# Optimization experiments

Measured on AMD Instinct MI355X. Metric: run time of the kernel, lower is better.

The kernel has to match this reference:

```python
import jax, jax.numpy as jnp
import numpy as np

B, S, D, H = 512, 512, 64, 128  # batch, seq_len, input_size, hidden_size


def setup_inputs() -> dict:
    key = jax.random.key(0)
    ks = jax.random.split(key, 12)
    s_in = 1.0 / np.sqrt(H)
    def u(k, shape):
        return jax.random.uniform(k, shape, jnp.float32, -s_in, s_in)
    return {
        "x": jax.random.normal(ks[0], (B, S, D), jnp.float32),
        # layer 0 (PyTorch gate order i,f,g,o stacked along first dim)
        "W_ih0": u(ks[1], (4 * H, D)),
        "W_hh0": u(ks[2], (4 * H, H)),
        "b_ih0": u(ks[3], (4 * H,)),
        "b_hh0": u(ks[4], (4 * H,)),
        # layer 1
        "W_ih1": u(ks[5], (4 * H, H)),
        "W_hh1": u(ks[6], (4 * H, H)),
        "b_ih1": u(ks[7], (4 * H,)),
        "b_hh1": u(ks[8], (4 * H,)),
        # linear head hidden -> 1
        "W_lin": u(ks[9], (1, H)),
        "b_lin": u(ks[10], (1,)),
    }


def _lstm_layer(x, W_ih, W_hh, b_ih, b_hh):
    # x: [B, S, Din] -> h sequence [B, S, H]
    b, s, _ = x.shape
    h_dim = W_hh.shape[1]
    # precompute input contribution for all timesteps (the compute-heavy GEMM)
    pre = jnp.einsum('bsd,gd->bsg', x, W_ih) + (b_ih + b_hh)  # [B, S, 4H]

    def step(carry, p_t):
        h, c = carry
        gates = p_t + h @ W_hh.T  # [B, 4H]
        i, f, g, o = jnp.split(gates, 4, axis=-1)
        i = jax.nn.sigmoid(i)
        f = jax.nn.sigmoid(f)
        g = jnp.tanh(g)
        o = jax.nn.sigmoid(o)
        c = f * c + i * g
        h = o * jnp.tanh(c)
        return (h, c), h

    h0 = jnp.zeros((b, h_dim), x.dtype)
    (_, _), hs = jax.lax.scan(step, (h0, h0), pre.transpose(1, 0, 2))
    return hs.transpose(1, 0, 2)  # [B, S, H]


def reference(x, W_ih0, W_hh0, b_ih0, b_hh0, W_ih1, W_hh1, b_ih1, b_hh1, W_lin, b_lin):
    h1 = _lstm_layer(x, W_ih0, W_hh0, b_ih0, b_hh0)
    h2 = _lstm_layer(h1, W_ih1, W_hh1, b_ih1, b_hh1)
    last = h2[:, -1, :]  # [B, H]
    return last @ W_lin.T + b_lin  # [B, 1]
```

## Files before the change

kernel.cpp:

```cpp
#include <hip/hip_runtime.h>

typedef _Float16 half8 __attribute__((ext_vector_type(8)));
typedef _Float16 half4 __attribute__((ext_vector_type(4)));
typedef _Float16 half2v __attribute__((ext_vector_type(2)));
typedef float floatx4 __attribute__((ext_vector_type(4)));

__device__ __forceinline__ float fast_rcp(float x) { return __builtin_amdgcn_rcpf(x); }
__device__ __forceinline__ float fast_sigmoid(float x) {
  return fast_rcp(1.f + __expf(-x));
}
__device__ __forceinline__ float fast_tanh(float x) {
  return 1.f - 2.f * fast_rcp(1.f + __expf(2.f * x));
}

__global__ void prep_kernel(const float* __restrict__ wih0, const float* __restrict__ whh0,
                            const float* __restrict__ bih0, const float* __restrict__ bhh0,
                            const float* __restrict__ wih1, const float* __restrict__ whh1,
                            const float* __restrict__ bih1, const float* __restrict__ bhh1,
                            _Float16* __restrict__ w0f, _Float16* __restrict__ w1f,
                            float* __restrict__ bias0, float* __restrict__ bias1)
{
  int stride = gridDim.x * blockDim.x;
  int idx0 = blockIdx.x * blockDim.x + threadIdx.x;
  const int N0 = 6*32*64*8;
  const int N1 = 8*32*64*8;
  for (int e = idx0; e < N0 + N1 + 1024; e += stride) {
    if (e < N0) {
      int j = e & 7; int le = e >> 3; int lane = le & 63; int frag = le >> 6;
      int kt = frag >> 5, ntile = frag & 31;
      int n = ntile*16 + (lane & 15);
      int kk = kt*32 + ((lane >> 4) << 3) + j;
      float v = (kk < 64) ? wih0[n*64 + kk] : whh0[n*128 + (kk - 64)];
      w0f[e] = (_Float16)v;
    } else if (e < N0 + N1) {
      int e2 = e - N0;
      int j = e2 & 7; int le = e2 >> 3; int lane = le & 63; int frag = le >> 6;
      int kt = frag >> 5, ntile = frag & 31;
      int n = ntile*16 + (lane & 15);
      int kk = kt*32 + ((lane >> 4) << 3) + j;
      float v = (kk < 128) ? wih1[n*128 + kk] : whh1[n*128 + (kk - 128)];
      w1f[e2] = (_Float16)v;
    } else {
      int i = e - (N0 + N1);
      if (i < 512) bias0[i] = bih0[i] + bhh0[i];
      else         bias1[i - 512] = bih1[i - 512] + bhh1[i - 512];
    }
  }
}


__global__ __launch_bounds__(512, 2) void lstm_l0(const float* __restrict__ x,
    const _Float16* __restrict__ w0f, const float* __restrict__ bias0,
    _Float16* __restrict__ h1out)
{
  const int tid = threadIdx.x;
  const int lane = tid & 63;
  const int w = tid >> 6;
  const int r0 = blockIdx.x * 2;

  __shared__ float preLDS[2][8192];
  __shared__ half8 aF[2][2*64];
  __shared__ half8 hA[2][4*8];
  __shared__ _Float16 hist[16][2][128];

  for (int i = tid; i < 2*4*8*4; i += 512) ((int*)hA)[i] = 0;

  half8 bf[6][4];
#pragma unroll
  for (int kt = 0; kt < 6; ++kt)
#pragma unroll
    for (int g = 0; g < 4; ++g) {
      int frag = kt*32 + (g*8 + w);
      bf[kt][g] = *reinterpret_cast<const half8*>(w0f + (size_t)(frag*64 + lane)*8);
      asm volatile("" : "+a"(bf[kt][g]));
    }
  float bias_v[4];
#pragma unroll
  for (int g = 0; g < 4; ++g) bias_v[g] = bias0[g*128 + w*16 + (lane & 15)];

  const int sdt = tid >> 6, sr = (tid >> 5) & 1, scp = (tid & 31) * 2;
  const int sm = sdt*2 + sr;
  const int sidx = ((scp>>5)*64 + sm + (((scp&31)>>3)<<4))*8 + (scp & 7);

  const bool arow = (lane & 11) == 0;
  const int cIdx = ((lane >> 4) << 1) | ((lane >> 2) & 1);
  const int rb = lane >> 4;
  const int en = w*16 + (lane & 15);
  const int eoff = ((en>>5)*8 + ((en&31)>>3)*2 + rb)*8 + (en&7);
  float cst = 0.f;

  {
    float2 v0 = *reinterpret_cast<const float2*>(x + ((size_t)(r0+sr)*512 + sdt)*64 + scp);
    float2 v1 = *reinterpret_cast<const float2*>(x + ((size_t)(r0+sr)*512 + 8 + sdt)*64 + scp);
    half2v h0; h0[0] = (_Float16)v0.x; h0[1] = (_Float16)v0.y;
    half2v h1v; h1v[0] = (_Float16)v1.x; h1v[1] = (_Float16)v1.y;
    *reinterpret_cast<half2v*>(((_Float16*)aF[0]) + sidx) = h0;
    *reinterpret_cast<half2v*>(((_Float16*)aF[1]) + sidx) = h1v;
  }
  __syncthreads();
  {
    floatx4 accP[4];
#pragma unroll
    for (int g = 0; g < 4; ++g) { float bb = bias_v[g]; accP[g] = (floatx4){bb,bb,bb,bb}; }
#pragma unroll
    for (int kt = 0; kt < 2; ++kt) {
      half8 af = aF[0][kt*64 + lane];
#pragma unroll
      for (int g = 0; g < 4; ++g)
        accP[g] = __builtin_amdgcn_mfma_f32_16x16x32_f16(af, bf[kt][g], accP[g], 0, 0, 0);
    }
#pragma unroll
    for (int reg = 0; reg < 4; ++reg) {
      int m = ((lane>>4)<<2) + reg;
      floatx4 pv = (floatx4){accP[0][reg], accP[1][reg], accP[2][reg], accP[3][reg]};
      *reinterpret_cast<floatx4*>(&preLDS[0][(m*128 + en)*4]) = pv;
    }
  }
  __syncthreads();

  half8 a2 = {}, a3 = {}, a4 = {}, a5 = {};

  for (int t = 0; t < 512; ++t) {
    const int b = t >> 3;
    if ((t & 7) == 0 && b < 62) {
      int s = (b+2)*8 + sdt;
      float2 v = *reinterpret_cast<const float2*>(x + ((size_t)(r0+sr)*512 + s)*64 + scp);
      half2v hv; hv[0] = (_Float16)v.x; hv[1] = (_Float16)v.y;
      *reinterpret_cast<half2v*>(((_Float16*)aF[b&1]) + sidx) = hv;
    }
    __syncthreads();
    if ((t & 7) == 0) {
      if (t != 0) {
        int tbase = t - 8;
        int fr = tid >> 8, rest = tid & 255;
        int fdt = rest >> 5, n = (rest & 31) * 4;
        half4 v = *reinterpret_cast<const half4*>(&hist[(tbase + fdt) & 15][fr][n]);
        *reinterpret_cast<half4*>(h1out + ((size_t)(r0 + fr)*512 + tbase + fdt)*128 + n) = v;
      }
      if (b < 63) {
        int slot = (b+1) & 1;
        floatx4 accP[4];
#pragma unroll
        for (int g = 0; g < 4; ++g) { float bb = bias_v[g]; accP[g] = (floatx4){bb,bb,bb,bb}; }
#pragma unroll
        for (int kt = 0; kt < 2; ++kt) {
          half8 af = aF[slot][kt*64 + lane];
#pragma unroll
          for (int g = 0; g < 4; ++g)
            accP[g] = __builtin_amdgcn_mfma_f32_16x16x32_f16(af, bf[kt][g], accP[g], 0, 0, 0);
        }
#pragma unroll
        for (int reg = 0; reg < 4; ++reg) {
          int m = ((lane>>4)<<2) + reg;
          floatx4 pv = (floatx4){accP[0][reg], accP[1][reg], accP[2][reg], accP[3][reg]};
          *reinterpret_cast<floatx4*>(&preLDS[slot][(m*128 + en)*4]) = pv;
        }
      }
    }

    floatx4 p4 = (floatx4){0.f, 0.f, 0.f, 0.f};
    if (lane < 32) {
      int mstep = ((t & 7) << 1) + rb;
      p4 = *reinterpret_cast<const floatx4*>(&preLDS[b & 1][(mstep*128 + en)*4]);
    }
    floatx4 acc[4];
#pragma unroll
    for (int g = 0; g < 4; ++g) acc[g] = (floatx4){p4[g], 0.f, 0.f, 0.f};

    const int cur = t & 1;
    if (arow) {
      a2 = hA[cur][0*8 + cIdx];
      a3 = hA[cur][1*8 + cIdx];
      a4 = hA[cur][2*8 + cIdx];
      a5 = hA[cur][3*8 + cIdx];
    }
#pragma unroll
    for (int g = 0; g < 4; ++g)
      acc[g] = __builtin_amdgcn_mfma_f32_16x16x32_f16(a2, bf[2][g], acc[g], 0, 0, 0);
#pragma unroll
    for (int g = 0; g < 4; ++g)
      acc[g] = __builtin_amdgcn_mfma_f32_16x16x32_f16(a3, bf[3][g], acc[g], 0, 0, 0);
#pragma unroll
    for (int g = 0; g < 4; ++g)
      acc[g] = __builtin_amdgcn_mfma_f32_16x16x32_f16(a4, bf[4][g], acc[g], 0, 0, 0);
#pragma unroll
    for (int g = 0; g < 4; ++g)
      acc[g] = __builtin_amdgcn_mfma_f32_16x16x32_f16(a5, bf[5][g], acc[g], 0, 0, 0);

    if (lane < 32) {
      float ii = fast_sigmoid(acc[0][0]);
      float ff = fast_sigmoid(acc[1][0]);
      float gg = fast_tanh(acc[2][0]);
      float oo = fast_sigmoid(acc[3][0]);
      cst = ff*cst + ii*gg;
      float hv2 = oo*fast_tanh(cst);
      _Float16 hh = (_Float16)hv2;
      ((_Float16*)hA[cur^1])[eoff] = hh;
      hist[t & 15][rb][en] = hh;
    }
  }
  __syncthreads();
  {
    int tbase = 504;
    int fr = tid >> 8, rest = tid & 255;
    int fdt = rest >> 5, n = (rest & 31) * 4;
    half4 v = *reinterpret_cast<const half4*>(&hist[(tbase + fdt) & 15][fr][n]);
    *reinterpret_cast<half4*>(h1out + ((size_t)(r0 + fr)*512 + tbase + fdt)*128 + n) = v;
  }
}

__global__ __launch_bounds__(512, 2) void lstm_l1(const _Float16* __restrict__ h1in,
    const _Float16* __restrict__ w1f, const float* __restrict__ bias1,
    const float* __restrict__ wlin, const float* __restrict__ blin,
    float* __restrict__ out)
{
  const int tid = threadIdx.x;
  const int lane = tid & 63;
  const int w = tid >> 6;
  const int r0 = blockIdx.x * 2;

  __shared__ float preLDS[2][8192];
  __shared__ half8 aF[2][4*64];
  __shared__ half8 hA[2][4*8];
  __shared__ float head[256];

  for (int i = tid; i < 2*4*8*4; i += 512) ((int*)hA)[i] = 0;

  half8 bf[8][4];
#pragma unroll
  for (int kt = 0; kt < 8; ++kt)
#pragma unroll
    for (int g = 0; g < 4; ++g) {
      int frag = kt*32 + (g*8 + w);
      bf[kt][g] = *reinterpret_cast<const half8*>(w1f + (size_t)(frag*64 + lane)*8);
      asm volatile("" : "+a"(bf[kt][g]));
    }
  float bias_v[4];
#pragma unroll
  for (int g = 0; g < 4; ++g) bias_v[g] = bias1[g*128 + w*16 + (lane & 15)];

  const int sdt = tid >> 6, sr = (tid >> 5) & 1, scq = (tid & 31) * 4;
  const int sm = sdt*2 + sr;
  const int sidx = ((scq>>5)*64 + sm + (((scq&31)>>3)<<4))*8 + (scq & 7);

  const bool arow = (lane & 11) == 0;
  const int cIdx = ((lane >> 4) << 1) | ((lane >> 2) & 1);
  const int rb = lane >> 4;
  const int en = w*16 + (lane & 15);
  const int eoff = ((en>>5)*8 + ((en&31)>>3)*2 + rb)*8 + (en&7);
  const float wl = (lane < 32) ? wlin[en] : 0.f;
  float cst = 0.f;
  float hl = 0.f;

  {
    uint2 v0 = *reinterpret_cast<const uint2*>(h1in + ((size_t)(r0+sr)*512 + sdt)*128 + scq);
    uint2 v1 = *reinterpret_cast<const uint2*>(h1in + ((size_t)(r0+sr)*512 + 8 + sdt)*128 + scq);
    *reinterpret_cast<uint2*>(((_Float16*)aF[0]) + sidx) = v0;
    *reinterpret_cast<uint2*>(((_Float16*)aF[1]) + sidx) = v1;
  }
  __syncthreads();
  {
    floatx4 accP[4];
#pragma unroll
    for (int g = 0; g < 4; ++g) { float bb = bias_v[g]; accP[g] = (floatx4){bb,bb,bb,bb}; }
#pragma unroll
    for (int kt = 0; kt < 4; ++kt) {
      half8 af = aF[0][kt*64 + lane];
#pragma unroll
      for (int g = 0; g < 4; ++g)
        accP[g] = __builtin_amdgcn_mfma_f32_16x16x32_f16(af, bf[kt][g], accP[g], 0, 0, 0);
    }
#pragma unroll
    for (int reg = 0; reg < 4; ++reg) {
      int m = ((lane>>4)<<2) + reg;
      floatx4 pv = (floatx4){accP[0][reg], accP[1][reg], accP[2][reg], accP[3][reg]};
      *reinterpret_cast<floatx4*>(&preLDS[0][(m*128 + en)*4]) = pv;
    }
  }
  __syncthreads();

  half8 a4 = {}, a5 = {}, a6 = {}, a7 = {};

  for (int t = 0; t < 512; ++t) {
    const int b = t >> 3;
    if ((t & 7) == 0 && b < 62) {
      int s = (b+2)*8 + sdt;
      uint2 v = *reinterpret_cast<const uint2*>(h1in + ((size_t)(r0+sr)*512 + s)*128 + scq);
      *reinterpret_cast<uint2*>(((_Float16*)aF[b&1]) + sidx) = v;
    }
    __syncthreads();
    if ((t & 7) == 0 && b < 63) {
      int slot = (b+1) & 1;
      floatx4 accP[4];
#pragma unroll
      for (int g = 0; g < 4; ++g) { float bb = bias_v[g]; accP[g] = (floatx4){bb,bb,bb,bb}; }
#pragma unroll
      for (int kt = 0; kt < 4; ++kt) {
        half8 af = aF[slot][kt*64 + lane];
#pragma unroll
        for (int g = 0; g < 4; ++g)
          accP[g] = __builtin_amdgcn_mfma_f32_16x16x32_f16(af, bf[kt][g], accP[g], 0, 0, 0);
      }
#pragma unroll
      for (int reg = 0; reg < 4; ++reg) {
        int m = ((lane>>4)<<2) + reg;
        floatx4 pv = (floatx4){accP[0][reg], accP[1][reg], accP[2][reg], accP[3][reg]};
        *reinterpret_cast<floatx4*>(&preLDS[slot][(m*128 + en)*4]) = pv;
      }
    }

    floatx4 p4 = (floatx4){0.f, 0.f, 0.f, 0.f};
    if (lane < 32) {
      int mstep = ((t & 7) << 1) + rb;
      p4 = *reinterpret_cast<const floatx4*>(&preLDS[b & 1][(mstep*128 + en)*4]);
    }
    floatx4 acc[4];
#pragma unroll
    for (int g = 0; g < 4; ++g) acc[g] = (floatx4){p4[g], 0.f, 0.f, 0.f};

    const int cur = t & 1;
    if (arow) {
      a4 = hA[cur][0*8 + cIdx];
      a5 = hA[cur][1*8 + cIdx];
      a6 = hA[cur][2*8 + cIdx];
      a7 = hA[cur][3*8 + cIdx];
    }
#pragma unroll
    for (int g = 0; g < 4; ++g)
      acc[g] = __builtin_amdgcn_mfma_f32_16x16x32_f16(a4, bf[4][g], acc[g], 0, 0, 0);
#pragma unroll
    for (int g = 0; g < 4; ++g)
      acc[g] = __builtin_amdgcn_mfma_f32_16x16x32_f16(a5, bf[5][g], acc[g], 0, 0, 0);
#pragma unroll
    for (int g = 0; g < 4; ++g)
      acc[g] = __builtin_amdgcn_mfma_f32_16x16x32_f16(a6, bf[6][g], acc[g], 0, 0, 0);
#pragma unroll
    for (int g = 0; g < 4; ++g)
      acc[g] = __builtin_amdgcn_mfma_f32_16x16x32_f16(a7, bf[7][g], acc[g], 0, 0, 0);

    if (lane < 32) {
      float ii = fast_sigmoid(acc[0][0]);
      float ff = fast_sigmoid(acc[1][0]);
      float gg = fast_tanh(acc[2][0]);
      float oo = fast_sigmoid(acc[3][0]);
      cst = ff*cst + ii*gg;
      hl = oo*fast_tanh(cst);
      ((_Float16*)hA[cur^1])[eoff] = (_Float16)hl;
    }
  }

  if (lane < 32) head[rb*128 + en] = hl * wl;
  __syncthreads();
  if (tid < 2) {
    float s = blin[0];
    for (int n = 0; n < 128; ++n) s += head[tid*128 + n];
    out[r0 + tid] = s;
  }
}

extern "C" void kernel_launch(void* const* d_in, const int* in_sizes, int n_in,
                              void* d_out, int out_size, void* d_ws, size_t ws_size,
                              hipStream_t stream)
{
  const float* x    = (const float*)d_in[0];
  const float* wih0 = (const float*)d_in[1];
  const float* whh0 = (const float*)d_in[2];
  const float* bih0 = (const float*)d_in[3];
  const float* bhh0 = (const float*)d_in[4];
  const float* wih1 = (const float*)d_in[5];
  const float* whh1 = (const float*)d_in[6];
  const float* bih1 = (const float*)d_in[7];
  const float* bhh1 = (const float*)d_in[8];
  const float* wlin = (const float*)d_in[9];
  const float* blin = (const float*)d_in[10];
  float* out = (float*)d_out;

  char* ws = (char*)d_ws;
  _Float16* w0f = (_Float16*)(ws);
  _Float16* w1f = (_Float16*)(ws + 196608);
  float* bias0  = (float*)(ws + 458752);
  float* bias1  = (float*)(ws + 460800);
  _Float16* h1  = (_Float16*)(ws + 1048576);

  prep_kernel<<<256, 256, 0, stream>>>(wih0, whh0, bih0, bhh0, wih1, whh1, bih1, bhh1,
                                       w0f, w1f, bias0, bias1);
  lstm_l0<<<256, 512, 0, stream>>>(x, w0f, bias0, h1);
  lstm_l1<<<256, 512, 0, stream>>>(h1, w1f, bias1, wlin, blin, out);
}
```

Measured before the change: 785.2 us.

## Unroll LSTM recurrence by 16 steps with compile-time slots and prefetched loads

The per-timestep loop in both LSTM layer kernels is restructured into windows of 8 steps, unrolled two at a time, so buffer slots and history indices become compile-time constants. The precomputed input-gate row for the next step is loaded from LDS early, before the activations, instead of at the start of each step. The global load of the next input chunk is issued before the window's compute and written to LDS only after a later barrier, hiding load latency behind the recurrence. Code size and register pressure grow, and the barrier placement changes the ordering of LDS writes and reads.

```diff
diff --git a/kernel.cpp b/kernel.cpp
--- a/kernel.cpp
+++ b/kernel.cpp
@@ -4,6 +4,8 @@
 typedef _Float16 half4 __attribute__((ext_vector_type(4)));
 typedef _Float16 half2v __attribute__((ext_vector_type(2)));
 typedef float floatx4 __attribute__((ext_vector_type(4)));
+
+template<int N> struct ic { static constexpr int value = N; };
 
 __device__ __forceinline__ float fast_rcp(float x) { return __builtin_amdgcn_rcpf(x); }
 __device__ __forceinline__ float fast_sigmoid(float x) {
@@ -48,7 +50,6 @@
   }
 }
 
-
 __global__ __launch_bounds__(512, 2) void lstm_l0(const float* __restrict__ x,
     const _Float16* __restrict__ w0f, const float* __restrict__ bias0,
     _Float16* __restrict__ h1out)
@@ -87,6 +88,8 @@
   const int rb = lane >> 4;
   const int en = w*16 + (lane & 15);
   const int eoff = ((en>>5)*8 + ((en&31)>>3)*2 + rb)*8 + (en&7);
+  const int fr = tid >> 8, rest = tid & 255;
+  const int fdt = rest >> 5, fn = (rest & 31) * 4;
   float cst = 0.f;
 
   {
@@ -116,78 +119,43 @@
       *reinterpret_cast<floatx4*>(&preLDS[0][(m*128 + en)*4]) = pv;
     }
   }
-  __syncthreads();
 
   half8 a2 = {}, a3 = {}, a4 = {}, a5 = {};
-
-  for (int t = 0; t < 512; ++t) {
-    const int b = t >> 3;
-    if ((t & 7) == 0 && b < 62) {
-      int s = (b+2)*8 + sdt;
-      float2 v = *reinterpret_cast<const float2*>(x + ((size_t)(r0+sr)*512 + s)*64 + scp);
-      half2v hv; hv[0] = (_Float16)v.x; hv[1] = (_Float16)v.y;
-      *reinterpret_cast<half2v*>(((_Float16*)aF[b&1]) + sidx) = hv;
-    }
-    __syncthreads();
-    if ((t & 7) == 0) {
-      if (t != 0) {
-        int tbase = t - 8;
-        int fr = tid >> 8, rest = tid & 255;
-        int fdt = rest >> 5, n = (rest & 31) * 4;
-        half4 v = *reinterpret_cast<const half4*>(&hist[(tbase + fdt) & 15][fr][n]);
-        *reinterpret_cast<half4*>(h1out + ((size_t)(r0 + fr)*512 + tbase + fdt)*128 + n) = v;
-      }
-      if (b < 63) {
-        int slot = (b+1) & 1;
-        floatx4 accP[4];
-#pragma unroll
-        for (int g = 0; g < 4; ++g) { float bb = bias_v[g]; accP[g] = (floatx4){bb,bb,bb,bb}; }
-#pragma unroll
-        for (int kt = 0; kt < 2; ++kt) {
-          half8 af = aF[slot][kt*64 + lane];
-#pragma unroll
-          for (int g = 0; g < 4; ++g)
-            accP[g] = __builtin_amdgcn_mfma_f32_16x16x32_f16(af, bf[kt][g], accP[g], 0, 0, 0);
-        }
-#pragma unroll
-        for (int reg = 0; reg < 4; ++reg) {
-          int m = ((lane>>4)<<2) + reg;
-          floatx4 pv = (floatx4){accP[0][reg], accP[1][reg], accP[2][reg], accP[3][reg]};
-          *reinterpret_cast<floatx4*>(&preLDS[slot][(m*128 + en)*4]) = pv;
-        }
-      }
-    }
-
-    floatx4 p4 = (floatx4){0.f, 0.f, 0.f, 0.f};
+  float2 sv;
+  floatx4 acc[4];
+#pragma unroll
+  for (int g = 0; g < 4; ++g) acc[g] = (floatx4){0.f,0.f,0.f,0.f};
+
+  floatx4 p4c = (floatx4){0.f,0.f,0.f,0.f};
+  if (lane < 32)
+    p4c = *reinterpret_cast<const floatx4*>(&preLDS[0][(rb*128 + en)*4]);
+
+  auto core = [&](auto tag) {
+    constexpr int TM = decltype(tag)::value;
+    constexpr int CUR = TM & 1;
+    constexpr int TN = (TM + 1) & 15;
+    if (arow) {
+      a2 = hA[CUR][ 0 + cIdx];
+      a3 = hA[CUR][ 8 + cIdx];
+      a4 = hA[CUR][16 + cIdx];
+      a5 = hA[CUR][24 + cIdx];
+    }
+    acc[0][0] = p4c[0]; acc[1][0] = p4c[1]; acc[2][0] = p4c[2]; acc[3][0] = p4c[3];
+#pragma unroll
+    for (int g = 0; g < 4; ++g)
+      acc[g] = __builtin_amdgcn_mfma_f32_16x16x32_f16(a2, bf[2][g], acc[g], 0, 0, 0);
+#pragma unroll
+    for (int g = 0; g < 4; ++g)
+      acc[g] = __builtin_amdgcn_mfma_f32_16x16x32_f16(a3, bf[3][g], acc[g], 0, 0, 0);
+#pragma unroll
+    for (int g = 0; g < 4; ++g)
+      acc[g] = __builtin_amdgcn_mfma_f32_16x16x32_f16(a4, bf[4][g], acc[g], 0, 0, 0);
+#pragma unroll
+    for (int g = 0; g < 4; ++g)
+      acc[g] = __builtin_amdgcn_mfma_f32_16x16x32_f16(a5, bf[5][g], acc[g], 0, 0, 0);
     if (lane < 32) {
-      int mstep = ((t & 7) << 1) + rb;
-      p4 = *reinterpret_cast<const floatx4*>(&preLDS[b & 1][(mstep*128 + en)*4]);
-    }
-    floatx4 acc[4];
-#pragma unroll
-    for (int g = 0; g < 4; ++g) acc[g] = (floatx4){p4[g], 0.f, 0.f, 0.f};
-
-    const int cur = t & 1;
-    if (arow) {
-      a2 = hA[cur][0*8 + cIdx];
-      a3 = hA[cur][1*8 + cIdx];
-      a4 = hA[cur][2*8 + cIdx];
-      a5 = hA[cur][3*8 + cIdx];
-    }
-#pragma unroll
-    for (int g = 0; g < 4; ++g)
-      acc[g] = __builtin_amdgcn_mfma_f32_16x16x32_f16(a2, bf[2][g], acc[g], 0, 0, 0);
-#pragma unroll
-    for (int g = 0; g < 4; ++g)
-      acc[g] = __builtin_amdgcn_mfma_f32_16x16x32_f16(a3, bf[3][g], acc[g], 0, 0, 0);
-#pragma unroll
-    for (int g = 0; g < 4; ++g)
-      acc[g] = __builtin_amdgcn_mfma_f32_16x16x32_f16(a4, bf[4][g], acc[g], 0, 0, 0);
-#pragma unroll
-    for (int g = 0; g < 4; ++g)
-      acc[g] = __builtin_amdgcn_mfma_f32_16x16x32_f16(a5, bf[5][g], acc[g], 0, 0, 0);
-
-    if (lane < 32) {
+      p4c = *reinterpret_cast<const floatx4*>(
+          &preLDS[TN >> 3][((((TN & 7) << 1) + rb)*128 + en)*4]);
       float ii = fast_sigmoid(acc[0][0]);
       float ff = fast_sigmoid(acc[1][0]);
       float gg = fast_tanh(acc[2][0]);
@@ -195,17 +163,62 @@
       cst = ff*cst + ii*gg;
       float hv2 = oo*fast_tanh(cst);
       _Float16 hh = (_Float16)hv2;
-      ((_Float16*)hA[cur^1])[eoff] = hh;
-      hist[t & 15][rb][en] = hh;
-    }
+      ((_Float16*)hA[CUR^1])[eoff] = hh;
+      hist[TM][rb][en] = hh;
+    }
+  };
+
+  auto window = [&](int B, auto slot_tag) {
+    constexpr int SLOT = decltype(slot_tag)::value;
+    __syncthreads();
+    if (B < 62)
+      sv = *reinterpret_cast<const float2*>(x + ((size_t)(r0+sr)*512 + (B+2)*8 + sdt)*64 + scp);
+    if (B >= 1) {
+      int tbase = (B-1)*8;
+      half4 v = *reinterpret_cast<const half4*>(&hist[((SLOT^1)<<3) + fdt][fr][fn]);
+      *reinterpret_cast<half4*>(h1out + ((size_t)(r0+fr)*512 + tbase + fdt)*128 + fn) = v;
+    }
+    if (B < 63) {
+      floatx4 accP[4];
+#pragma unroll
+      for (int g = 0; g < 4; ++g) { float bb = bias_v[g]; accP[g] = (floatx4){bb,bb,bb,bb}; }
+#pragma unroll
+      for (int kt = 0; kt < 2; ++kt) {
+        half8 af = aF[SLOT^1][kt*64 + lane];
+#pragma unroll
+        for (int g = 0; g < 4; ++g)
+          accP[g] = __builtin_amdgcn_mfma_f32_16x16x32_f16(af, bf[kt][g], accP[g], 0, 0, 0);
+      }
+#pragma unroll
+      for (int reg = 0; reg < 4; ++reg) {
+        int m = ((lane>>4)<<2) + reg;
+        floatx4 pv = (floatx4){accP[0][reg], accP[1][reg], accP[2][reg], accP[3][reg]};
+        *reinterpret_cast<floatx4*>(&preLDS[SLOT^1][(m*128 + en)*4]) = pv;
+      }
+    }
+    core(ic<SLOT*8 + 0>{});
+    __syncthreads();
+    if (B < 62) {
+      half2v hv; hv[0] = (_Float16)sv.x; hv[1] = (_Float16)sv.y;
+      *reinterpret_cast<half2v*>(((_Float16*)aF[SLOT]) + sidx) = hv;
+    }
+    core(ic<SLOT*8 + 1>{});
+    __syncthreads(); core(ic<SLOT*8 + 2>{});
+    __syncthreads(); core(ic<SLOT*8 + 3>{});
+    __syncthreads(); core(ic<SLOT*8 + 4>{});
+    __syncthreads(); core(ic<SLOT*8 + 5>{});
+    __syncthreads(); core(ic<SLOT*8 + 6>{});
+    __syncthreads(); core(ic<SLOT*8 + 7>{});
+  };
+
+  for (int bp = 0; bp < 32; ++bp) {
+    window(2*bp,     ic<0>{});
+    window(2*bp + 1, ic<1>{});
   }
   __syncthreads();
   {
-    int tbase = 504;
-    int fr = tid >> 8, rest = tid & 255;
-    int fdt = rest >> 5, n = (rest & 31) * 4;
-    half4 v = *reinterpret_cast<const half4*>(&hist[(tbase + fdt) & 15][fr][n]);
-    *reinterpret_cast<half4*>(h1out + ((size_t)(r0 + fr)*512 + tbase + fdt)*128 + n) = v;
+    half4 v = *reinterpret_cast<const half4*>(&hist[8 + fdt][fr][fn]);
+    *reinterpret_cast<half4*>(h1out + ((size_t)(r0+fr)*512 + 504 + fdt)*128 + fn) = v;
   }
 }
 
@@ -277,76 +290,92 @@
       *reinterpret_cast<floatx4*>(&preLDS[0][(m*128 + en)*4]) = pv;
     }
   }
-  __syncthreads();
 
   half8 a4 = {}, a5 = {}, a6 = {}, a7 = {};
-
-  for (int t = 0; t < 512; ++t) {
-    const int b = t >> 3;
-    if ((t & 7) == 0 && b < 62) {
-      int s = (b+2)*8 + sdt;
-      uint2 v = *reinterpret_cast<const uint2*>(h1in + ((size_t)(r0+sr)*512 + s)*128 + scq);
-      *reinterpret_cast<uint2*>(((_Float16*)aF[b&1]) + sidx) = v;
-    }
-    __syncthreads();
-    if ((t & 7) == 0 && b < 63) {
-      int slot = (b+1) & 1;
-      floatx4 accP[4];
-#pragma unroll
-      for (int g = 0; g < 4; ++g) { float bb = bias_v[g]; accP[g] = (floatx4){bb,bb,bb,bb}; }
-#pragma unroll
-      for (int kt = 0; kt < 4; ++kt) {
-        half8 af = aF[slot][kt*64 + lane];
-#pragma unroll
-        for (int g = 0; g < 4; ++g)
-          accP[g] = __builtin_amdgcn_mfma_f32_16x16x32_f16(af, bf[kt][g], accP[g], 0, 0, 0);
-      }
-#pragma unroll
-      for (int reg = 0; reg < 4; ++reg) {
-        int m = ((lane>>4)<<2) + reg;
-        floatx4 pv = (floatx4){accP[0][reg], accP[1][reg], accP[2][reg], accP[3][reg]};
-        *reinterpret_cast<floatx4*>(&preLDS[slot][(m*128 + en)*4]) = pv;
-      }
-    }
-
-    floatx4 p4 = (floatx4){0.f, 0.f, 0.f, 0.f};
+  uint2 sv;
+  floatx4 acc[4];
+#pragma unroll
+  for (int g = 0; g < 4; ++g) acc[g] = (floatx4){0.f,0.f,0.f,0.f};
+
+  floatx4 p4c = (floatx4){0.f,0.f,0.f,0.f};
+  if (lane < 32)
+    p4c = *reinterpret_cast<const floatx4*>(&preLDS[0][(rb*128 + en)*4]);
+
+  auto core = [&](auto tag) {
+    constexpr int TM = decltype(tag)::value;
+    constexpr int CUR = TM & 1;
+    constexpr int TN = (TM + 1) & 15;
+    if (arow) {
+      a4 = hA[CUR][ 0 + cIdx];
+      a5 = hA[CUR][ 8 + cIdx];
+      a6 = hA[CUR][16 + cIdx];
+      a7 = hA[CUR][24 + cIdx];
+    }
+    acc[0][0] = p4c[0]; acc[1][0] = p4c[1]; acc[2][0] = p4c[2]; acc[3][0] = p4c[3];
+#pragma unroll
+    for (int g = 0; g < 4; ++g)
+      acc[g] = __builtin_amdgcn_mfma_f32_16x16x32_f16(a4, bf[4][g], acc[g], 0, 0, 0);
+#pragma unroll
+    for (int g = 0; g < 4; ++g)
+      acc[g] = __builtin_amdgcn_mfma_f32_16x16x32_f16(a5, bf[5][g], acc[g], 0, 0, 0);
+#pragma unroll
+    for (int g = 0; g < 4; ++g)
+      acc[g] = __builtin_amdgcn_mfma_f32_16x16x32_f16(a6, bf[6][g], acc[g], 0, 0, 0);
+#pragma unroll
+    for (int g = 0; g < 4; ++g)
+      acc[g] = __builtin_amdgcn_mfma_f32_16x16x32_f16(a7, bf[7][g], acc[g], 0, 0, 0);
     if (lane < 32) {
-      int mstep = ((t & 7) << 1) + rb;
-      p4 = *reinterpret_cast<const floatx4*>(&preLDS[b & 1][(mstep*128 + en)*4]);
-    }
-    floatx4 acc[4];
-#pragma unroll
-    for (int g = 0; g < 4; ++g) acc[g] = (floatx4){p4[g], 0.f, 0.f, 0.f};
-
-    const int cur = t & 1;
-    if (arow) {
-      a4 = hA[cur][0*8 + cIdx];
-      a5 = hA[cur][1*8 + cIdx];
-      a6 = hA[cur][2*8 + cIdx];
-      a7 = hA[cur][3*8 + cIdx];
-    }
-#pragma unroll
-    for (int g = 0; g < 4; ++g)
-      acc[g] = __builtin_amdgcn_mfma_f32_16x16x32_f16(a4, bf[4][g], acc[g], 0, 0, 0);
-#pragma unroll
-    for (int g = 0; g < 4; ++g)
-      acc[g] = __builtin_amdgcn_mfma_f32_16x16x32_f16(a5, bf[5][g], acc[g], 0, 0, 0);
-#pragma unroll
-    for (int g = 0; g < 4; ++g)
-      acc[g] = __builtin_amdgcn_mfma_f32_16x16x32_f16(a6, bf[6][g], acc[g], 0, 0, 0);
-#pragma unroll
-    for (int g = 0; g < 4; ++g)
-      acc[g] = __builtin_amdgcn_mfma_f32_16x16x32_f16(a7, bf[7][g], acc[g], 0, 0, 0);
-
-    if (lane < 32) {
+      p4c = *reinterpret_cast<const floatx4*>(
+          &preLDS[TN >> 3][((((TN & 7) << 1) + rb)*128 + en)*4]);
       float ii = fast_sigmoid(acc[0][0]);
       float ff = fast_sigmoid(acc[1][0]);
       float gg = fast_tanh(acc[2][0]);
       float oo = fast_sigmoid(acc[3][0]);
       cst = ff*cst + ii*gg;
       hl = oo*fast_tanh(cst);
-      ((_Float16*)hA[cur^1])[eoff] = (_Float16)hl;
-    }
+      ((_Float16*)hA[CUR^1])[eoff] = (_Float16)hl;
+    }
+  };
+
+  auto window = [&](int B, auto slot_tag) {
+    constexpr int SLOT = decltype(slot_tag)::value;
+    __syncthreads();
+    if (B < 62)
+      sv = *reinterpret_cast<const uint2*>(h1in + ((size_t)(r0+sr)*512 + (B+2)*8 + sdt)*128 + scq);
+    if (B < 63) {
+      floatx4 accP[4];
+#pragma unroll
+      for (int g = 0; g < 4; ++g) { float bb = bias_v[g]; accP[g] = (floatx4){bb,bb,bb,bb}; }
+#pragma unroll
+      for (int kt = 0; kt < 4; ++kt) {
+        half8 af = aF[SLOT^1][kt*64 + lane];
+#pragma unroll
+        for (int g = 0; g < 4; ++g)
+          accP[g] = __builtin_amdgcn_mfma_f32_16x16x32_f16(af, bf[kt][g], accP[g], 0, 0, 0);
+      }
+#pragma unroll
+      for (int reg = 0; reg < 4; ++reg) {
+        int m = ((lane>>4)<<2) + reg;
+        floatx4 pv = (floatx4){accP[0][reg], accP[1][reg], accP[2][reg], accP[3][reg]};
+        *reinterpret_cast<floatx4*>(&preLDS[SLOT^1][(m*128 + en)*4]) = pv;
+      }
+    }
+    core(ic<SLOT*8 + 0>{});
+    __syncthreads();
+    if (B < 62)
+      *reinterpret_cast<uint2*>(((_Float16*)aF[SLOT]) + sidx) = sv;
+    core(ic<SLOT*8 + 1>{});
+    __syncthreads(); core(ic<SLOT*8 + 2>{});
+    __syncthreads(); core(ic<SLOT*8 + 3>{});
+    __syncthreads(); core(ic<SLOT*8 + 4>{});
+    __syncthreads(); core(ic<SLOT*8 + 5>{});
+    __syncthreads(); core(ic<SLOT*8 + 6>{});
+    __syncthreads(); core(ic<SLOT*8 + 7>{});
+  };
+
+  for (int bp = 0; bp < 32; ++bp) {
+    window(2*bp,     ic<0>{});
+    window(2*bp + 1, ic<1>{});
   }
 
   if (lane < 32) head[rb*128 + en] = hl * wl;
```

After: 674.4 us (median of 2 runs). 14.1% less time.
